# Kernel tuning notes

Measured on AMD Instinct MI355X. Metric: run time of the kernel, lower is better.

## Reference

```python
import jax, jax.numpy as jnp
from jax import lax
import numpy as np

B, T, H31, W = 16, 96, 31, 64
C1, C2, LH, NC = 16, 32, 64, 10

def _conv(x, w, b):
    # NCHW conv, 3x3, padding=1 ('SAME'), fused bias + relu
    y = lax.conv_general_dilated(x, w, (1, 1), 'SAME', dimension_numbers=('NCHW', 'OIHW', 'NCHW'))
    return jax.nn.relu(y + b[None, :, None, None])

def _lstm(xs, w_ih, w_hh, b):
    # xs: [T, B, D]; PyTorch gate order i, f, g, o
    Hd = w_hh.shape[1]
    def step(carry, x):
        h, c = carry
        g = x @ w_ih.T + h @ w_hh.T + b
        i, f, gg, o = jnp.split(g, 4, -1)
        c = jax.nn.sigmoid(f) * c + jax.nn.sigmoid(i) * jnp.tanh(gg)
        h = jax.nn.sigmoid(o) * jnp.tanh(c)
        return (h, c), h
    z = jnp.zeros((xs.shape[1], Hd), xs.dtype)
    _, hs = lax.scan(step, (z, z), xs)
    return hs  # [T, B, H]

def setup_inputs():
    key = jax.random.key(0)
    ks = jax.random.split(key, 26)
    n = lambda i, shape, s=0.1: jax.random.normal(ks[i], shape, jnp.float32) * s
    return {
        'x_real': jax.random.normal(ks[0], (B, T, H31, W), jnp.float32),
        'x_imag': jax.random.normal(ks[1], (B, T, H31, W), jnp.float32),
        'lengths': jax.random.randint(ks[2], (B,), 1, T + 1),
        'conv1r_w': n(3, (C1, 1, 3, 3), 0.3), 'conv1r_b': n(4, (C1,)),
        'conv1i_w': n(5, (C1, 1, 3, 3), 0.3), 'conv1i_b': n(6, (C1,)),
        'conv2r_w': n(7, (C2, C1, 3, 3), 0.15), 'conv2r_b': n(8, (C2,)),
        'conv2i_w': n(9, (C2, C1, 3, 3), 0.15), 'conv2i_b': n(10, (C2,)),
        'fus_w': n(11, (2 * C2, 4 * C2), 0.1), 'fus_b': n(12, (2 * C2,)),
        'wf_ih': n(13, (4 * LH, 2 * C2), 0.1), 'wf_hh': n(14, (4 * LH, LH), 0.1),
        'bf_ih': n(15, (4 * LH,)), 'bf_hh': n(16, (4 * LH,)),
        'wb_ih': n(17, (4 * LH, 2 * C2), 0.1), 'wb_hh': n(18, (4 * LH, LH), 0.1),
        'bb_ih': n(19, (4 * LH,)), 'bb_hh': n(20, (4 * LH,)),
        'fc_w': n(21, (NC, 2 * LH), 0.1), 'fc_b': n(22, (NC,)),
    }

def reference(x_real, x_imag, lengths, conv1r_w, conv1r_b, conv1i_w, conv1i_b, conv2r_w, conv2r_b, conv2i_w, conv2i_b, fus_w, fus_b, wf_ih, wf_hh, bf_ih, bf_hh, wb_ih, wb_hh, bb_ih, bb_hh, fc_w, fc_b):
    Bb, Tt, Hh, Ww = x_real.shape
    # batch all (sample, timestep) conv work together: [B*T, 1, 31, W]
    xr = x_real.reshape(Bb * Tt, 1, Hh, Ww)
    xi = x_imag.reshape(Bb * Tt, 1, Hh, Ww)
    rf = _conv(_conv(xr, conv1r_w, conv1r_b), conv2r_w, conv2r_b)
    mf = _conv(_conv(xi, conv1i_w, conv1i_b), conv2i_w, conv2i_b)
    r = rf.mean((-2, -1))  # AdaptiveAvgPool2d((1,1)) -> [B*T, C2]
    m = mf.mean((-2, -1))
    mag = jnp.sqrt(r * r + m * m)           # abs(r + 1j*m)
    ang = jnp.arctan2(m, r)                 # angle(r + 1j*m)
    feat = jnp.concatenate([r, m, mag, ang], -1)  # [B*T, 4*C2]
    fused = jax.nn.relu(feat @ fus_w.T + fus_b).reshape(Bb, Tt, -1)  # dropout = identity (eval)
    # forward LSTM: output at t < length is unaffected by padded steps
    hs_f = _lstm(fused.transpose(1, 0, 2), wf_ih, wf_hh, bf_ih + bf_hh)  # [T, B, LH]
    last_f = hs_f[lengths - 1, jnp.arange(Bb)]
    # backward LSTM over length-reversed sequence (packed-sequence semantics)
    rev_idx = jnp.clip(lengths[:, None] - 1 - jnp.arange(Tt)[None, :], 0, Tt - 1)  # [B, T]
    x_rev = jnp.take_along_axis(fused, rev_idx[:, :, None], axis=1)
    hs_b = _lstm(x_rev.transpose(1, 0, 2), wb_ih, wb_hh, bb_ih + bb_hh)
    # backward hidden at original position length-1 is the first reverse step
    last = jnp.concatenate([last_f, hs_b[0]], -1)  # [B, 2*LH]
    return last @ fc_w.T + fc_b
```

## Files before the change

### kernel.cpp

```cpp
#include <hip/hip_runtime.h>
#include <math.h>

#define BB 16
#define TT 96
#define HH 31
#define WW 64
#define BT (BB*TT)
#define C1 16
#define C2 32
#define LH 64
#define NC 10

typedef _Float16 half8 __attribute__((ext_vector_type(8)));
typedef float floatx16 __attribute__((ext_vector_type(16)));

#define XPAD 66
#define YPAD 33
#define NPOS (YPAD*XPAD)
#define SXBYTES (NPOS*32 + 128)

__device__ __forceinline__ int swz(int byte) {
    return byte ^ (((byte >> 7) & 7) << 4);
}

__global__ __launch_bounds__(512, 2)
void conv_pool_mfma(const float* __restrict__ xr, const float* __restrict__ xi,
                    const float* __restrict__ w1r, const float* __restrict__ b1r,
                    const float* __restrict__ w1i, const float* __restrict__ b1i,
                    const float* __restrict__ w2r, const float* __restrict__ b2r,
                    const float* __restrict__ w2i, const float* __restrict__ b2i,
                    float* __restrict__ pool_r, float* __restrict__ pool_m)
{
    __shared__ __align__(128) unsigned char s_x[SXBYTES];
    __shared__ float s_pool[C2];

    const int tid  = threadIdx.x;
    const int lane = tid & 63;
    const int img  = blockIdx.x;
    const int part = blockIdx.y;

    const float* xg = (part ? xi : xr) + img*(HH*WW);
    const float* w1 = part ? w1i : w1r;
    const float* b1 = part ? b1i : b1r;
    const float* w2 = part ? w2i : w2r;
    const float* b2 = part ? b2i : b2r;
    float* poolo = (part ? pool_m : pool_r) + img*C2;

    if (tid < C2) s_pool[tid] = 0.f;

    if (tid < 194) {
        int pos;
        if (tid < 66)       pos = tid;
        else if (tid < 132) pos = 32*XPAD + (tid - 66);
        else {
            int i = tid - 132;
            pos = (1 + (i >> 1))*XPAD + ((i & 1) ? 65 : 0);
        }
        *reinterpret_cast<int4*>(s_x + swz(pos*32))      = make_int4(0,0,0,0);
        *reinterpret_cast<int4*>(s_x + swz(pos*32 + 16)) = make_int4(0,0,0,0);
    }

    if (tid < HH*16) {
        const int y  = tid >> 4;
        const int x0 = (tid & 15) << 2;
        float patch[3][6];
        #pragma unroll
        for (int ky = 0; ky < 3; ++ky) {
            int row = y + ky - 1;
            #pragma unroll
            for (int j = 0; j < 6; ++j) {
                int col = x0 + j - 1;
                patch[ky][j] = (row >= 0 && row < HH && col >= 0 && col < WW)
                                 ? xg[row*WW + col] : 0.f;
            }
        }
        #pragma unroll
        for (int p = 0; p < 2; ++p) {
            float acc[8][4];
            #pragma unroll
            for (int ch = 0; ch < 8; ++ch) {
                float bb = b1[p*8 + ch];
                #pragma unroll
                for (int j = 0; j < 4; ++j) acc[ch][j] = bb;
            }
            #pragma unroll
            for (int ky = 0; ky < 3; ++ky)
                #pragma unroll
                for (int kx = 0; kx < 3; ++kx) {
                    #pragma unroll
                    for (int ch = 0; ch < 8; ++ch) {
                        float wv = w1[(p*8 + ch)*9 + ky*3 + kx];
                        #pragma unroll
                        for (int j = 0; j < 4; ++j)
                            acc[ch][j] += patch[ky][kx + j] * wv;
                    }
                }
            #pragma unroll
            for (int j = 0; j < 4; ++j) {
                half8 v;
                #pragma unroll
                for (int ch = 0; ch < 8; ++ch)
                    v[ch] = (_Float16)fmaxf(acc[ch][j], 0.f);
                int pos = (y + 1)*XPAD + (x0 + j + 1);
                *reinterpret_cast<half8*>(s_x + swz(pos*32 + p*16)) = v;
            }
        }
    }

    const int oc  = lane & 31;
    const int icb = (lane >> 5) * 8;
    half8 af[9];
    #pragma unroll
    for (int t = 0; t < 9; ++t) {
        half8 v;
        #pragma unroll
        for (int i = 0; i < 8; ++i)
            v[i] = (_Float16)w2[(oc*C1 + icb + i)*9 + t];
        af[t] = v;
    }
    float bias[16];
    #pragma unroll
    for (int r = 0; r < 16; ++r)
        bias[r] = b2[(r & 3) + 8*(r >> 2) + 4*(lane >> 5)];

    __syncthreads();

    float pool[16];
    #pragma unroll
    for (int r = 0; r < 16; ++r) pool[r] = 0.f;

    const int wav = tid >> 6;
    const int halfoff = (lane >> 5) << 4;

    #define LDB(dst, ky, kx) do { \
        int byte_ = (pbase + (ky)*XPAD + (kx))*32 + halfoff; \
        dst = *reinterpret_cast<const half8*>(s_x + swz(byte_)); } while (0)

    for (int tile = wav; tile < 62; tile += 8) {
        int y  = tile >> 1;
        int x0 = (tile & 1) * 32;
        int pbase = y*XPAD + x0 + (lane & 31);
        floatx16 acc;
        #pragma unroll
        for (int r = 0; r < 16; ++r) acc[r] = bias[r];

        half8 r0a, r0b, r0c, r1a, r1b, r1c, r2a, r2b, r2c;
        LDB(r0a, 0, 0); LDB(r0b, 0, 1); LDB(r0c, 0, 2);
        LDB(r1a, 1, 0); LDB(r1b, 1, 1); LDB(r1c, 1, 2);
        acc = __builtin_amdgcn_mfma_f32_32x32x16_f16(af[0], r0a, acc, 0, 0, 0);
        acc = __builtin_amdgcn_mfma_f32_32x32x16_f16(af[1], r0b, acc, 0, 0, 0);
        acc = __builtin_amdgcn_mfma_f32_32x32x16_f16(af[2], r0c, acc, 0, 0, 0);
        LDB(r2a, 2, 0); LDB(r2b, 2, 1); LDB(r2c, 2, 2);
        acc = __builtin_amdgcn_mfma_f32_32x32x16_f16(af[3], r1a, acc, 0, 0, 0);
        acc = __builtin_amdgcn_mfma_f32_32x32x16_f16(af[4], r1b, acc, 0, 0, 0);
        acc = __builtin_amdgcn_mfma_f32_32x32x16_f16(af[5], r1c, acc, 0, 0, 0);
        acc = __builtin_amdgcn_mfma_f32_32x32x16_f16(af[6], r2a, acc, 0, 0, 0);
        acc = __builtin_amdgcn_mfma_f32_32x32x16_f16(af[7], r2b, acc, 0, 0, 0);
        acc = __builtin_amdgcn_mfma_f32_32x32x16_f16(af[8], r2c, acc, 0, 0, 0);

        #pragma unroll
        for (int r = 0; r < 16; ++r) pool[r] += fmaxf(acc[r], 0.f);
    }
    #undef LDB

    #pragma unroll
    for (int m = 1; m <= 16; m <<= 1) {
        #pragma unroll
        for (int r = 0; r < 16; ++r) pool[r] += __shfl_xor(pool[r], m, 64);
    }
    if ((lane & 31) == 0) {
        #pragma unroll
        for (int r = 0; r < 16; ++r)
            atomicAdd(&s_pool[(r & 3) + 8*(r >> 2) + 4*(lane >> 5)], pool[r]);
    }
    __syncthreads();
    if (tid < C2) poolo[tid] = s_pool[tid] * (1.f/1984.f);
}

__device__ __forceinline__ float sigm(float x){ return 1.f/(1.f + __expf(-x)); }
__device__ __forceinline__ float ftanh(float x){
    float xc = fminf(fmaxf(x, -15.f), 15.f);
    float e = __expf(2.f*xc);
    return (e - 1.f)/(e + 1.f);
}

__global__ __launch_bounds__(512, 1)
void lstm_fused(const float* __restrict__ pool_r, const float* __restrict__ pool_m,
                const int* __restrict__ lengths,
                const float* __restrict__ fus_w, const float* __restrict__ fus_b,
                const float* __restrict__ wf_ih, const float* __restrict__ wf_hh,
                const float* __restrict__ bf_ih, const float* __restrict__ bf_hh,
                const float* __restrict__ wb_ih, const float* __restrict__ wb_hh,
                const float* __restrict__ bb_ih, const float* __restrict__ bb_hh,
                float* __restrict__ last_f, float* __restrict__ hb0)
{
    __shared__ __align__(16) float s_gx[TT*256];
    __shared__ __align__(16) float s_fused[TT][64];
    __shared__ float s_h[64];
    __shared__ float s_g[256];

    const int tid = threadIdx.x;
    const int b   = blockIdx.x & 15;
    const bool bwd = blockIdx.x >= 16;
    const int len = lengths[b];

    if (!bwd) {
        for (int i = tid; i < TT*32; i += 512) {
            int t = i >> 5, c = i & 31;
            float r = pool_r[(b*TT + t)*C2 + c];
            float m = pool_m[(b*TT + t)*C2 + c];
            float* f = s_gx + t*128;
            f[c]      = r;
            f[32 + c] = m;
            f[64 + c] = sqrtf(r*r + m*m);
            f[96 + c] = atan2f(m, r);
        }
        __syncthreads();

        {
            const int k = tid & 63, tq = tid >> 6;
            float4 wreg[32];
            #pragma unroll
            for (int q = 0; q < 32; ++q)
                wreg[q] = *reinterpret_cast<const float4*>(fus_w + k*128 + q*4);
            const float bk = fus_b[k];
            for (int j = 0; j < 12; ++j) {
                int t = tq*12 + j;
                const float* f = s_gx + t*128;
                float a0=0.f, a1=0.f, a2=0.f, a3=0.f;
                #pragma unroll
                for (int q = 0; q < 32; ++q) {
                    float4 fv = *reinterpret_cast<const float4*>(f + q*4);
                    a0 += wreg[q].x*fv.x; a1 += wreg[q].y*fv.y;
                    a2 += wreg[q].z*fv.z; a3 += wreg[q].w*fv.w;
                }
                s_fused[t][k] = fmaxf((a0+a1) + (a2+a3) + bk, 0.f);
            }
        }
        __syncthreads();

        {
            const int g = tid & 255, th = tid >> 8;
            float wih[64];
            #pragma unroll
            for (int q = 0; q < 64; q += 4) {
                float4 a = *reinterpret_cast<const float4*>(wf_ih + g*64 + q);
                wih[q]=a.x; wih[q+1]=a.y; wih[q+2]=a.z; wih[q+3]=a.w;
            }
            const float bg = bf_ih[g] + bf_hh[g];
            for (int j = 0; j < 48; ++j) {
                int t = th*48 + j;
                float a0=0.f, a1=0.f, a2=0.f, a3=0.f;
                #pragma unroll
                for (int q = 0; q < 64; q += 4) {
                    float4 fv = *reinterpret_cast<const float4*>(&s_fused[t][q]);
                    a0 += wih[q]*fv.x;   a1 += wih[q+1]*fv.y;
                    a2 += wih[q+2]*fv.z; a3 += wih[q+3]*fv.w;
                }
                s_gx[t*256 + g] = (a0+a1) + (a2+a3) + bg;
            }
        }
        __syncthreads();

        const int g = tid & 255;
        float whh[64];
        #pragma unroll
        for (int q = 0; q < 64; q += 4) {
            float4 a = *reinterpret_cast<const float4*>(wf_hh + g*64 + q);
            whh[q]=a.x; whh[q+1]=a.y; whh[q+2]=a.z; whh[q+3]=a.w;
        }
        if (tid < 64) s_h[tid] = 0.f;
        __syncthreads();
        float creg = 0.f;
        for (int t = 0; t < TT; ++t) {
            if (tid < 256) {
                float a0=0.f, a1=0.f, a2=0.f, a3=0.f;
                #pragma unroll
                for (int q = 0; q < 64; q += 4) {
                    float4 hv = *reinterpret_cast<const float4*>(&s_h[q]);
                    a0 += whh[q]*hv.x;   a1 += whh[q+1]*hv.y;
                    a2 += whh[q+2]*hv.z; a3 += whh[q+3]*hv.w;
                }
                s_g[g] = (a0+a1) + (a2+a3) + s_gx[t*256 + g];
            }
            __syncthreads();
            if (tid < 64) {
                float iv = sigm(s_g[tid]);
                float fv = sigm(s_g[64+tid]);
                float gv = ftanh(s_g[128+tid]);
                float ov = sigm(s_g[192+tid]);
                creg = fv*creg + iv*gv;
                float h = ov*ftanh(creg);
                s_h[tid] = h;
                if (t == len-1) last_f[b*64+tid] = h;
            }
            __syncthreads();
        }
    } else {
        const int t0 = len - 1;
        if (tid < 32) {
            int c = tid;
            float r = pool_r[(b*TT + t0)*C2 + c];
            float m = pool_m[(b*TT + t0)*C2 + c];
            s_gx[c]      = r;
            s_gx[32 + c] = m;
            s_gx[64 + c] = sqrtf(r*r + m*m);
            s_gx[96 + c] = atan2f(m, r);
        }
        __syncthreads();
        if (tid < 64) {
            float acc = fus_b[tid];
            const float4* wv = reinterpret_cast<const float4*>(fus_w + tid*128);
            #pragma unroll
            for (int q = 0; q < 32; ++q) {
                float4 w = wv[q];
                float4 f = *reinterpret_cast<const float4*>(s_gx + q*4);
                acc += w.x*f.x + w.y*f.y + w.z*f.z + w.w*f.w;
            }
            s_fused[0][tid] = fmaxf(acc, 0.f);
        }
        __syncthreads();
        if (tid < 256) {
            float acc = bb_ih[tid] + bb_hh[tid];
            const float4* wv = reinterpret_cast<const float4*>(wb_ih + tid*64);
            #pragma unroll
            for (int q = 0; q < 16; ++q) {
                float4 w = wv[q];
                float4 f = *reinterpret_cast<const float4*>(&s_fused[0][q*4]);
                acc += w.x*f.x + w.y*f.y + w.z*f.z + w.w*f.w;
            }
            s_g[tid] = acc;
        }
        __syncthreads();
        if (tid < 64) {
            float iv = sigm(s_g[tid]);
            float gv = ftanh(s_g[128+tid]);
            float ov = sigm(s_g[192+tid]);
            float c = iv*gv;
            hb0[b*64+tid] = ov*ftanh(c);
        }
    }
}

__global__ __launch_bounds__(256)
void final_fc_kernel(const float* __restrict__ last_f, const float* __restrict__ hb0,
                     const float* __restrict__ fc_w, const float* __restrict__ fc_b,
                     float* __restrict__ out)
{
    int t = threadIdx.x;
    if (t >= BB*NC) return;
    int b = t / NC, k = t % NC;
    float acc = fc_b[k];
    const float* w = fc_w + k*128;
    #pragma unroll
    for (int j = 0; j < 64; ++j) acc += last_f[b*64+j]*w[j];
    #pragma unroll
    for (int j = 0; j < 64; ++j) acc += hb0[b*64+j]*w[64+j];
    out[b*NC + k] = acc;
}

extern "C" void kernel_launch(void* const* d_in, const int* in_sizes, int n_in,
                              void* d_out, int out_size, void* d_ws, size_t ws_size,
                              hipStream_t stream)
{
    const float* x_real = (const float*)d_in[0];
    const float* x_imag = (const float*)d_in[1];
    const int*   lengths= (const int*)d_in[2];
    const float* c1r_w = (const float*)d_in[3];
    const float* c1r_b = (const float*)d_in[4];
    const float* c1i_w = (const float*)d_in[5];
    const float* c1i_b = (const float*)d_in[6];
    const float* c2r_w = (const float*)d_in[7];
    const float* c2r_b = (const float*)d_in[8];
    const float* c2i_w = (const float*)d_in[9];
    const float* c2i_b = (const float*)d_in[10];
    const float* fus_w = (const float*)d_in[11];
    const float* fus_b = (const float*)d_in[12];
    const float* wf_ih = (const float*)d_in[13];
    const float* wf_hh = (const float*)d_in[14];
    const float* bf_ih = (const float*)d_in[15];
    const float* bf_hh = (const float*)d_in[16];
    const float* wb_ih = (const float*)d_in[17];
    const float* wb_hh = (const float*)d_in[18];
    const float* bb_ih = (const float*)d_in[19];
    const float* bb_hh = (const float*)d_in[20];
    const float* fc_w  = (const float*)d_in[21];
    const float* fc_b  = (const float*)d_in[22];
    float* out = (float*)d_out;

    float* ws     = (float*)d_ws;
    float* pool_r = ws;
    float* pool_m = pool_r + BT*C2;
    float* last_f = pool_m + BT*C2;
    float* hb0    = last_f + BB*LH;

    conv_pool_mfma<<<dim3(BT, 2), 512, 0, stream>>>(
        x_real, x_imag, c1r_w, c1r_b, c1i_w, c1i_b,
        c2r_w, c2r_b, c2i_w, c2i_b, pool_r, pool_m);

    lstm_fused<<<32, 512, 0, stream>>>(pool_r, pool_m, lengths,
        fus_w, fus_b, wf_ih, wf_hh, bf_ih, bf_hh,
        wb_ih, wb_hh, bb_ih, bb_hh, last_f, hb0);

    final_fc_kernel<<<1, 256, 0, stream>>>(last_f, hb0, fc_w, fc_b, out);
}
```

Measured before the change: 347.4 us.

## Split LSTM into parallel input-projection kernel and shuffle-based recurrent scan

The fused LSTM kernel is split in two. A new prep kernel launches one block per (sample, timestep) to compute the fused features and the input-gate projections across the whole grid. The scan kernel then runs only the recurrence: gate values are exchanged with wave shuffles so every thread applies the nonlinearity, h is double-buffered so each step needs one barrier instead of two, and the next step's input gates are prefetched from global memory. This takes the serial projection work off the 16-block critical path, at the cost of an extra launch and a global round trip for the gates_x buffer.

```diff
diff --git a/kernel.cpp b/kernel.cpp
--- a/kernel.cpp
+++ b/kernel.cpp
@@ -184,160 +184,144 @@
     return (e - 1.f)/(e + 1.f);
 }
 
-__global__ __launch_bounds__(512, 1)
-void lstm_fused(const float* __restrict__ pool_r, const float* __restrict__ pool_m,
-                const int* __restrict__ lengths,
-                const float* __restrict__ fus_w, const float* __restrict__ fus_b,
-                const float* __restrict__ wf_ih, const float* __restrict__ wf_hh,
-                const float* __restrict__ bf_ih, const float* __restrict__ bf_hh,
-                const float* __restrict__ wb_ih, const float* __restrict__ wb_hh,
-                const float* __restrict__ bb_ih, const float* __restrict__ bb_hh,
-                float* __restrict__ last_f, float* __restrict__ hb0)
-{
-    __shared__ __align__(16) float s_gx[TT*256];
-    __shared__ __align__(16) float s_fused[TT][64];
-    __shared__ float s_h[64];
-    __shared__ float s_g[256];
-
+__global__ __launch_bounds__(256)
+void lstm_prep(const float* __restrict__ pool_r, const float* __restrict__ pool_m,
+               const float* __restrict__ fus_w, const float* __restrict__ fus_b,
+               const float* __restrict__ wf_ih,
+               const float* __restrict__ bf_ih, const float* __restrict__ bf_hh,
+               float* __restrict__ fusedg, float* __restrict__ gates_x)
+{
+    __shared__ __align__(16) float s_feat[128];
+    __shared__ __align__(16) float s_fused[64];
+    const int bt  = blockIdx.x;
+    const int tid = threadIdx.x;
+
+    if (tid < 32) {
+        float r = pool_r[bt*C2 + tid];
+        float m = pool_m[bt*C2 + tid];
+        s_feat[tid]      = r;
+        s_feat[32 + tid] = m;
+        s_feat[64 + tid] = sqrtf(r*r + m*m);
+        s_feat[96 + tid] = atan2f(m, r);
+    }
+    __syncthreads();
+
+    if (tid < 64) {
+        float acc = fus_b[tid];
+        const float4* wv = reinterpret_cast<const float4*>(fus_w + tid*128);
+        float a0=0.f, a1=0.f, a2=0.f, a3=0.f;
+        #pragma unroll
+        for (int q = 0; q < 32; ++q) {
+            float4 w = wv[q];
+            float4 f = *reinterpret_cast<const float4*>(s_feat + q*4);
+            a0 += w.x*f.x; a1 += w.y*f.y; a2 += w.z*f.z; a3 += w.w*f.w;
+        }
+        float v = fmaxf(acc + (a0+a1) + (a2+a3), 0.f);
+        s_fused[tid] = v;
+        fusedg[bt*64 + tid] = v;
+    }
+    __syncthreads();
+
+    {
+        float acc = bf_ih[tid] + bf_hh[tid];
+        const float4* wv = reinterpret_cast<const float4*>(wf_ih + tid*64);
+        float a0=0.f, a1=0.f, a2=0.f, a3=0.f;
+        #pragma unroll
+        for (int q = 0; q < 16; ++q) {
+            float4 w = wv[q];
+            float4 f = *reinterpret_cast<const float4*>(s_fused + q*4);
+            a0 += w.x*f.x; a1 += w.y*f.y; a2 += w.z*f.z; a3 += w.w*f.w;
+        }
+        gates_x[bt*256 + tid] = acc + (a0+a1) + (a2+a3);
+    }
+}
+
+__global__ __launch_bounds__(256, 1)
+void lstm_scan(const float* __restrict__ gates_x, const float* __restrict__ fusedg,
+               const int* __restrict__ lengths,
+               const float* __restrict__ wf_hh,
+               const float* __restrict__ wb_ih,
+               const float* __restrict__ bb_ih, const float* __restrict__ bb_hh,
+               float* __restrict__ last_f, float* __restrict__ hb0)
+{
     const int tid = threadIdx.x;
     const int b   = blockIdx.x & 15;
-    const bool bwd = blockIdx.x >= 16;
     const int len = lengths[b];
 
-    if (!bwd) {
-        for (int i = tid; i < TT*32; i += 512) {
-            int t = i >> 5, c = i & 31;
-            float r = pool_r[(b*TT + t)*C2 + c];
-            float m = pool_m[(b*TT + t)*C2 + c];
-            float* f = s_gx + t*128;
-            f[c]      = r;
-            f[32 + c] = m;
-            f[64 + c] = sqrtf(r*r + m*m);
-            f[96 + c] = atan2f(m, r);
-        }
+    if (blockIdx.x < 16) {
+        __shared__ __align__(16) float s_h[2][64];
+        const int ln = tid & 63;
+        const int w  = tid >> 6;
+        const int q  = ln >> 4;
+        const int u  = w*16 + (ln & 15);
+        const int g  = q*64 + u;
+
+        float whh[64];
+        #pragma unroll
+        for (int j = 0; j < 64; j += 4) {
+            float4 a = *reinterpret_cast<const float4*>(wf_hh + g*64 + j);
+            whh[j]=a.x; whh[j+1]=a.y; whh[j+2]=a.z; whh[j+3]=a.w;
+        }
+        if (q == 0) s_h[0][u] = 0.f;
         __syncthreads();
 
-        {
-            const int k = tid & 63, tq = tid >> 6;
-            float4 wreg[32];
-            #pragma unroll
-            for (int q = 0; q < 32; ++q)
-                wreg[q] = *reinterpret_cast<const float4*>(fus_w + k*128 + q*4);
-            const float bk = fus_b[k];
-            for (int j = 0; j < 12; ++j) {
-                int t = tq*12 + j;
-                const float* f = s_gx + t*128;
-                float a0=0.f, a1=0.f, a2=0.f, a3=0.f;
-                #pragma unroll
-                for (int q = 0; q < 32; ++q) {
-                    float4 fv = *reinterpret_cast<const float4*>(f + q*4);
-                    a0 += wreg[q].x*fv.x; a1 += wreg[q].y*fv.y;
-                    a2 += wreg[q].z*fv.z; a3 += wreg[q].w*fv.w;
-                }
-                s_fused[t][k] = fmaxf((a0+a1) + (a2+a3) + bk, 0.f);
-            }
-        }
-        __syncthreads();
-
-        {
-            const int g = tid & 255, th = tid >> 8;
-            float wih[64];
-            #pragma unroll
-            for (int q = 0; q < 64; q += 4) {
-                float4 a = *reinterpret_cast<const float4*>(wf_ih + g*64 + q);
-                wih[q]=a.x; wih[q+1]=a.y; wih[q+2]=a.z; wih[q+3]=a.w;
-            }
-            const float bg = bf_ih[g] + bf_hh[g];
-            for (int j = 0; j < 48; ++j) {
-                int t = th*48 + j;
-                float a0=0.f, a1=0.f, a2=0.f, a3=0.f;
-                #pragma unroll
-                for (int q = 0; q < 64; q += 4) {
-                    float4 fv = *reinterpret_cast<const float4*>(&s_fused[t][q]);
-                    a0 += wih[q]*fv.x;   a1 += wih[q+1]*fv.y;
-                    a2 += wih[q+2]*fv.z; a3 += wih[q+3]*fv.w;
-                }
-                s_gx[t*256 + g] = (a0+a1) + (a2+a3) + bg;
-            }
-        }
-        __syncthreads();
-
-        const int g = tid & 255;
-        float whh[64];
-        #pragma unroll
-        for (int q = 0; q < 64; q += 4) {
-            float4 a = *reinterpret_cast<const float4*>(wf_hh + g*64 + q);
-            whh[q]=a.x; whh[q+1]=a.y; whh[q+2]=a.z; whh[q+3]=a.w;
-        }
-        if (tid < 64) s_h[tid] = 0.f;
-        __syncthreads();
+        const float* gxp = gates_x + (b*TT)*256 + g;
+        float gx = gxp[0];
         float creg = 0.f;
         for (int t = 0; t < TT; ++t) {
-            if (tid < 256) {
-                float a0=0.f, a1=0.f, a2=0.f, a3=0.f;
-                #pragma unroll
-                for (int q = 0; q < 64; q += 4) {
-                    float4 hv = *reinterpret_cast<const float4*>(&s_h[q]);
-                    a0 += whh[q]*hv.x;   a1 += whh[q+1]*hv.y;
-                    a2 += whh[q+2]*hv.z; a3 += whh[q+3]*hv.w;
-                }
-                s_g[g] = (a0+a1) + (a2+a3) + s_gx[t*256 + g];
-            }
+            float gxn = (t+1 < TT) ? gxp[(t+1)*256] : 0.f;
+
+            const int cur = t & 1;
+            float a0=0.f, a1=0.f, a2=0.f, a3=0.f;
+            #pragma unroll
+            for (int j = 0; j < 64; j += 4) {
+                float4 hv = *reinterpret_cast<const float4*>(&s_h[cur][j]);
+                a0 += whh[j]*hv.x;   a1 += whh[j+1]*hv.y;
+                a2 += whh[j+2]*hv.z; a3 += whh[j+3]*hv.w;
+            }
+            float acc = gx + (a0+a1) + (a2+a3);
+
+            float p1 = __shfl_xor(acc, 16, 64);
+            float p2 = __shfl_xor(acc, 32, 64);
+            float p3 = __shfl_xor(p1,  32, 64);
+            float g0 = (q==0)?acc : (q==1)?p1 : (q==2)?p2 : p3;
+            float g1 = (q==1)?acc : (q==0)?p1 : (q==3)?p2 : p3;
+            float g2 = (q==2)?acc : (q==3)?p1 : (q==0)?p2 : p3;
+            float g3 = (q==3)?acc : (q==2)?p1 : (q==1)?p2 : p3;
+
+            creg = sigm(g1)*creg + sigm(g0)*ftanh(g2);
+            float h = sigm(g3)*ftanh(creg);
+
+            if (q == 0) {
+                s_h[cur^1][u] = h;
+                if (t == len-1) last_f[b*64 + u] = h;
+            }
+            gx = gxn;
             __syncthreads();
-            if (tid < 64) {
-                float iv = sigm(s_g[tid]);
-                float fv = sigm(s_g[64+tid]);
-                float gv = ftanh(s_g[128+tid]);
-                float ov = sigm(s_g[192+tid]);
-                creg = fv*creg + iv*gv;
-                float h = ov*ftanh(creg);
-                s_h[tid] = h;
-                if (t == len-1) last_f[b*64+tid] = h;
-            }
-            __syncthreads();
         }
     } else {
-        const int t0 = len - 1;
-        if (tid < 32) {
-            int c = tid;
-            float r = pool_r[(b*TT + t0)*C2 + c];
-            float m = pool_m[(b*TT + t0)*C2 + c];
-            s_gx[c]      = r;
-            s_gx[32 + c] = m;
-            s_gx[64 + c] = sqrtf(r*r + m*m);
-            s_gx[96 + c] = atan2f(m, r);
-        }
+        __shared__ __align__(16) float s_f[64];
+        __shared__ float s_g[256];
+        if (tid < 64) s_f[tid] = fusedg[(b*TT + (len-1))*64 + tid];
         __syncthreads();
-        if (tid < 64) {
-            float acc = fus_b[tid];
-            const float4* wv = reinterpret_cast<const float4*>(fus_w + tid*128);
-            #pragma unroll
-            for (int q = 0; q < 32; ++q) {
-                float4 w = wv[q];
-                float4 f = *reinterpret_cast<const float4*>(s_gx + q*4);
-                acc += w.x*f.x + w.y*f.y + w.z*f.z + w.w*f.w;
-            }
-            s_fused[0][tid] = fmaxf(acc, 0.f);
-        }
-        __syncthreads();
-        if (tid < 256) {
+        {
             float acc = bb_ih[tid] + bb_hh[tid];
             const float4* wv = reinterpret_cast<const float4*>(wb_ih + tid*64);
-            #pragma unroll
-            for (int q = 0; q < 16; ++q) {
-                float4 w = wv[q];
-                float4 f = *reinterpret_cast<const float4*>(&s_fused[0][q*4]);
-                acc += w.x*f.x + w.y*f.y + w.z*f.z + w.w*f.w;
-            }
-            s_g[tid] = acc;
+            float a0=0.f, a1=0.f, a2=0.f, a3=0.f;
+            #pragma unroll
+            for (int qq = 0; qq < 16; ++qq) {
+                float4 wvv = wv[qq];
+                float4 f = *reinterpret_cast<const float4*>(s_f + qq*4);
+                a0 += wvv.x*f.x; a1 += wvv.y*f.y; a2 += wvv.z*f.z; a3 += wvv.w*f.w;
+            }
+            s_g[tid] = acc + (a0+a1) + (a2+a3);
         }
         __syncthreads();
         if (tid < 64) {
             float iv = sigm(s_g[tid]);
             float gv = ftanh(s_g[128+tid]);
             float ov = sigm(s_g[192+tid]);
-            float c = iv*gv;
-            hb0[b*64+tid] = ov*ftanh(c);
+            hb0[b*64 + tid] = ov*ftanh(iv*gv);
         }
     }
 }
@@ -388,19 +372,23 @@
     const float* fc_b  = (const float*)d_in[22];
     float* out = (float*)d_out;
 
-    float* ws     = (float*)d_ws;
-    float* pool_r = ws;
-    float* pool_m = pool_r + BT*C2;
-    float* last_f = pool_m + BT*C2;
-    float* hb0    = last_f + BB*LH;
+    float* ws      = (float*)d_ws;
+    float* pool_r  = ws;
+    float* pool_m  = pool_r  + BT*C2;
+    float* fusedg  = pool_m  + BT*C2;
+    float* gates_x = fusedg  + BT*64;
+    float* last_f  = gates_x + BT*256;
+    float* hb0     = last_f  + BB*LH;
 
     conv_pool_mfma<<<dim3(BT, 2), 512, 0, stream>>>(
         x_real, x_imag, c1r_w, c1r_b, c1i_w, c1i_b,
         c2r_w, c2r_b, c2i_w, c2i_b, pool_r, pool_m);
 
-    lstm_fused<<<32, 512, 0, stream>>>(pool_r, pool_m, lengths,
-        fus_w, fus_b, wf_ih, wf_hh, bf_ih, bf_hh,
-        wb_ih, wb_hh, bb_ih, bb_hh, last_f, hb0);
+    lstm_prep<<<BT, 256, 0, stream>>>(pool_r, pool_m, fus_w, fus_b,
+                                      wf_ih, bf_ih, bf_hh, fusedg, gates_x);
+
+    lstm_scan<<<32, 256, 0, stream>>>(gates_x, fusedg, lengths, wf_hh,
+                                      wb_ih, bb_ih, bb_hh, last_f, hb0);
 
     final_fc_kernel<<<1, 256, 0, stream>>>(last_f, hb0, fc_w, fc_b, out);
 }
```

Measured after the change: 299.3 us. 13.8% less time.
